# Kernel tuning notes

Measured on AMD Instinct MI355X. Metric: run time of the kernel, lower is better.

Reference implementation:

```python
import jax, jax.numpy as jnp
import numpy as np

K_DIM = 64  # contraction dim for scores; scale = 1/sqrt(K_DIM)


def setup_inputs() -> dict:
    key = jax.random.key(0)
    ks = jax.random.split(key, 8)
    B, T, L, D, H, E, V = 128, 16, 32, 256, 8, 64, 64
    return {
        "queries": jax.random.normal(ks[0], (B, T, L, D), dtype=jnp.float32),
        "keys": jax.random.normal(ks[1], (B, T, L, D), dtype=jnp.float32),
        "values": jax.random.normal(ks[2], (B, T, L, D), dtype=jnp.float32),
        "attn_mask": jax.random.uniform(ks[3], (B, B), dtype=jnp.float32),
        "Wq": jax.random.normal(ks[4], (D, H, E), dtype=jnp.float32) * 0.05,
        "Wk": jax.random.normal(ks[5], (D, H, E), dtype=jnp.float32) * 0.05,
        "Wv": jax.random.normal(ks[6], (D, H, V), dtype=jnp.float32) * 0.05,
        "w_head": jax.random.normal(ks[7], (H,), dtype=jnp.float32),
    }


def reference(queries, keys, values, attn_mask, Wq, Wk, Wv, w_head):
    # QKV projections (EinsumDense 'abcd,def->abcef', no bias): [b,t,l,h,e]
    Q = jnp.einsum('btld,dhe->btlhe', queries, Wq)
    K = jnp.einsum('btld,dhe->btlhe', keys, Wk)
    V = jnp.einsum('btld,dhe->btlhe', values, Wv)

    scale = 1.0 / jnp.sqrt(jnp.float32(K_DIM))
    # cross-batch attention scores: [t, l, h, B, b]
    scores = jnp.einsum('Btlhe,btlhe->tlhBb', Q, K) * scale
    # multiplicative mask, broadcast over trailing [B, b]
    scores = scores * attn_mask
    # Dropout is identity at inference (Keras Dropout, training=False)

    attn = jnp.einsum('tlhBb,btlhe->Bthle', jax.nn.softmax(scores, axis=-1), V)
    # head-mixing output ('bthle,h->btle'): [b, t, l, v_dim]
    attn_output = jnp.einsum('bthle,h->btle', attn, w_head)
    return (attn_output, scores)
```

## Files before the change

### kernel.cpp

```cpp
#include <hip/hip_runtime.h>
#include <hip/hip_bf16.h>


using bf16x8 = __attribute__((ext_vector_type(8))) __bf16;
using f32x4  = __attribute__((ext_vector_type(4))) float;

__device__ __forceinline__ f32x4 mfma16(bf16x8 a, bf16x8 b, f32x4 c) {
  return __builtin_amdgcn_mfma_f32_16x16x32_bf16(a, b, c, 0, 0, 0);
}

__global__ __launch_bounds__(512) void k0_wt(const float* __restrict__ Wq,
                                             const float* __restrict__ Wk,
                                             const float* __restrict__ Wv,
                                             __bf16* __restrict__ Wt) {
  int f   = blockIdx.x * 512 + threadIdx.x;
  int mat = f >> 14;
  int rem = f & 16383;
  int d8  = rem >> 9;
  int col = rem & 511;
  const float* W = (mat == 0) ? Wq : (mat == 1) ? Wk : Wv;
  bf16x8 v;
#pragma unroll
  for (int i = 0; i < 8; ++i) v[i] = (__bf16)W[(d8 * 8 + i) * 512 + col];
  *(bf16x8*)(Wt + mat * 131072 + col * 256 + d8 * 8) = v;
}

__global__ __launch_bounds__(512) void k1_proj(const float* __restrict__ xq,
                                               const float* __restrict__ xk,
                                               const float* __restrict__ xv,
                                               const __bf16* __restrict__ Wt,
                                               __bf16* __restrict__ qkv) {
  __shared__ char smem[65536];
  const int tid  = threadIdx.x;
  const int tl   = blockIdx.x;
  const int m    = blockIdx.y;
  const int lane = tid & 63, w = tid >> 6;
  const int lrow = lane & 15, lk = lane >> 4;
  const f32x4 z4 = {0.f, 0.f, 0.f, 0.f};

  const float* xm = (m == 0) ? xq : (m == 1) ? xk : xv;

#pragma unroll
  for (int i = 0; i < 8; ++i) {
    int c = i * 512 + tid;
    int row = c >> 5, sl = c & 31;
    const float* g = xm + (size_t)row * 131072 + (size_t)tl * 256 + sl * 8;
    float4 f0 = *(const float4*)g;
    float4 f1 = *(const float4*)(g + 4);
    bf16x8 v;
    v[0] = (__bf16)f0.x; v[1] = (__bf16)f0.y; v[2] = (__bf16)f0.z; v[3] = (__bf16)f0.w;
    v[4] = (__bf16)f1.x; v[5] = (__bf16)f1.y; v[6] = (__bf16)f1.z; v[7] = (__bf16)f1.w;
    *(bf16x8*)(smem + row * 512 + ((sl ^ (row & 7)) << 4)) = v;
  }
  __syncthreads();

  const int h = w;
  const __bf16* wbase = Wt + (size_t)(m * 512 + h * 64) * 256;
  __bf16* dst = qkv + (size_t)(tl * 8 + h) * 32768 + m * 8192;

  for (int rh = 0; rh < 2; ++rh) {
    f32x4 acc[4][4];
#pragma unroll
    for (int ri = 0; ri < 4; ++ri)
#pragma unroll
      for (int ci = 0; ci < 4; ++ci) acc[ri][ci] = z4;

#pragma unroll
    for (int kk = 0; kk < 8; ++kk) {
      int koff = lk * 16 + kk * 64;
      bf16x8 a[4], b[4];
#pragma unroll
      for (int ri = 0; ri < 4; ++ri) {
        int row = rh * 64 + ri * 16 + lrow;
        a[ri] = *(const bf16x8*)(smem + row * 512 + (koff ^ ((row & 7) << 4)));
      }
#pragma unroll
      for (int ci = 0; ci < 4; ++ci)
        b[ci] = *(const bf16x8*)(wbase + (ci * 16 + lrow) * 256 + kk * 32 + lk * 8);
#pragma unroll
      for (int ri = 0; ri < 4; ++ri)
#pragma unroll
        for (int ci = 0; ci < 4; ++ci)
          acc[ri][ci] = mfma16(a[ri], b[ci], acc[ri][ci]);
    }

#pragma unroll
    for (int ri = 0; ri < 4; ++ri)
#pragma unroll
      for (int ci = 0; ci < 4; ++ci)
#pragma unroll
        for (int r = 0; r < 4; ++r) {
          int brow = rh * 64 + ri * 16 + lk * 4 + r;
          int e    = ci * 16 + lrow;
          dst[brow * 64 + e] = (__bf16)acc[ri][ci][r];
        }
  }
}

__global__ __launch_bounds__(512) void k2_attn(const float* __restrict__ mask,
                                               const float* __restrict__ w_head,
                                               float* out_base) {
  __shared__ char smem[81920];
  const int tid  = threadIdx.x;
  const int tl   = blockIdx.x;
  const int lane = tid & 63, w = tid >> 6;
  const int lrow = lane & 15, lk = lane >> 4;
  const f32x4 z4 = {0.f, 0.f, 0.f, 0.f};

  float* scores = out_base + 4194304;

  float mreg[8][4];
#pragma unroll
  for (int ct = 0; ct < 8; ++ct)
#pragma unroll
    for (int r = 0; r < 4; ++r)
      mreg[ct][r] = mask[(w * 16 + lk * 4 + r) * 128 + ct * 16 + lrow];

  f32x4 oacc[4];
#pragma unroll
  for (int i = 0; i < 4; ++i) oacc[i] = z4;

  for (int h = 0; h < 8; ++h) {
    const __bf16* slot = (const __bf16*)scores + (size_t)(tl * 8 + h) * 32768;
    float wh = w_head[h];
    __syncthreads();
#pragma unroll
    for (int i = 0; i < 2; ++i) {
      int c = i * 512 + tid;
      int row = c >> 3, sl = c & 7;
      uint4 qv = *(const uint4*)(slot + row * 64 + sl * 8);
      *(uint4*)(smem + row * 128 + ((sl ^ (row & 7)) << 4)) = qv;
      uint4 kv = *(const uint4*)(slot + 8192 + row * 64 + sl * 8);
      *(uint4*)(smem + 16384 + row * 128 + ((sl ^ (row & 7)) << 4)) = kv;
      bf16x8 vv = *(const bf16x8*)(slot + 16384 + row * 64 + sl * 8);
#pragma unroll
      for (int j = 0; j < 8; ++j) {
        int e = sl * 8 + j;
        *(__bf16*)(smem + 32768 + e * 256 + ((row * 2) ^ ((e & 7) << 4))) = vv[j];
      }
    }
    __syncthreads();

    int arow = w * 16 + lrow;
    const char* qb = smem + arow * 128;
    int aswz = (arow & 7) << 4;
    bf16x8 a0 = *(const bf16x8*)(qb + ((lk * 16 + 0) ^ aswz));
    bf16x8 a1 = *(const bf16x8*)(qb + ((lk * 16 + 64) ^ aswz));
    f32x4 sacc[8];
#pragma unroll
    for (int ct = 0; ct < 8; ++ct) {
      int bcol = ct * 16 + lrow;
      const char* kb = smem + 16384 + bcol * 128;
      int bswz = (bcol & 7) << 4;
      bf16x8 b0 = *(const bf16x8*)(kb + ((lk * 16 + 0) ^ bswz));
      bf16x8 b1 = *(const bf16x8*)(kb + ((lk * 16 + 64) ^ bswz));
      sacc[ct] = mfma16(a0, b0, z4);
      sacc[ct] = mfma16(a1, b1, sacc[ct]);
    }

    float* srow = scores + (size_t)(tl * 8 + h) * 16384;
#pragma unroll
    for (int ct = 0; ct < 8; ++ct)
#pragma unroll
      for (int r = 0; r < 4; ++r) {
        float s = sacc[ct][r] * 0.125f * mreg[ct][r];
        sacc[ct][r] = s;
        srow[(w * 16 + lk * 4 + r) * 128 + ct * 16 + lrow] = s;
      }

#pragma unroll
    for (int r = 0; r < 4; ++r) {
      float mx = sacc[0][r];
#pragma unroll
      for (int ct = 1; ct < 8; ++ct) mx = fmaxf(mx, sacc[ct][r]);
      mx = fmaxf(mx, __shfl_xor(mx, 1));
      mx = fmaxf(mx, __shfl_xor(mx, 2));
      mx = fmaxf(mx, __shfl_xor(mx, 4));
      mx = fmaxf(mx, __shfl_xor(mx, 8));
      float sum = 0.f;
#pragma unroll
      for (int ct = 0; ct < 8; ++ct) {
        float p = __expf(sacc[ct][r] - mx);
        sacc[ct][r] = p;
        sum += p;
      }
      sum += __shfl_xor(sum, 1);
      sum += __shfl_xor(sum, 2);
      sum += __shfl_xor(sum, 4);
      sum += __shfl_xor(sum, 8);
      float fct = wh / sum;
      int row16 = lk * 4 + r;
      char* pb = smem + 49152 + w * 4096 + row16 * 256;
      int pswz = (row16 & 7) << 4;
#pragma unroll
      for (int ct = 0; ct < 8; ++ct) {
        int col = ct * 16 + lrow;
        *(__bf16*)(pb + ((col * 2) ^ pswz)) = (__bf16)(sacc[ct][r] * fct);
      }
    }

    const char* pab = smem + 49152 + w * 4096 + lrow * 256;
    int paswz = (lrow & 7) << 4;
    bf16x8 pa[4];
#pragma unroll
    for (int kk = 0; kk < 4; ++kk)
      pa[kk] = *(const bf16x8*)(pab + ((lk * 16 + kk * 64) ^ paswz));
#pragma unroll
    for (int ct2 = 0; ct2 < 4; ++ct2) {
      int ecol = ct2 * 16 + lrow;
      const char* vb = smem + 32768 + ecol * 256;
      int vswz = (ecol & 7) << 4;
#pragma unroll
      for (int kk = 0; kk < 4; ++kk) {
        bf16x8 b = *(const bf16x8*)(vb + ((lk * 16 + kk * 64) ^ vswz));
        oacc[ct2] = mfma16(pa[kk], b, oacc[ct2]);
      }
    }
  }

#pragma unroll
  for (int ct2 = 0; ct2 < 4; ++ct2)
#pragma unroll
    for (int r = 0; r < 4; ++r) {
      int brow = w * 16 + lk * 4 + r;
      int e    = ct2 * 16 + lrow;
      out_base[(size_t)(brow * 512 + tl) * 64 + e] = oacc[ct2][r];
    }
}

extern "C" void kernel_launch(void* const* d_in, const int* in_sizes, int n_in,
                              void* d_out, int out_size, void* d_ws, size_t ws_size,
                              hipStream_t stream) {
  const float* q    = (const float*)d_in[0];
  const float* k    = (const float*)d_in[1];
  const float* v    = (const float*)d_in[2];
  const float* mask = (const float*)d_in[3];
  const float* Wq   = (const float*)d_in[4];
  const float* Wk   = (const float*)d_in[5];
  const float* Wv   = (const float*)d_in[6];
  const float* wh   = (const float*)d_in[7];
  float* out = (float*)d_out;

  __bf16* Wt  = (__bf16*)out;
  __bf16* qkv = (__bf16*)(out + 4194304);

  hipLaunchKernelGGL(k0_wt,   dim3(96),       dim3(512), 0, stream, Wq, Wk, Wv, Wt);
  hipLaunchKernelGGL(k1_proj, dim3(512, 3),   dim3(512), 0, stream, q, k, v, Wt, qkv);
  hipLaunchKernelGGL(k2_attn, dim3(512),      dim3(512), 0, stream, mask, wh, out);
}
```

Before: 235.2 us.

## Store V pre-transposed and vectorize projection writes, shrink attention LDS

The projection kernel is templated per matrix. For Q/K it swaps the MFMA operand order so each lane writes four contiguous bf16 values in one store, and for V it writes the output already transposed (e-major). The attention kernel then loads V with vectorized 16-byte copies instead of scalar transposing stores into LDS, and reads Q fragments straight from global memory, which cuts LDS from 80KB to 64KB. The one 2D launch becomes three separate launches, adding launch overhead, and launch_bounds(512,4) is added as an occupancy hint.

After: 323.6 us. +37.6%, slower.

```diff
diff --git a/kernel.cpp b/kernel.cpp
--- a/kernel.cpp
+++ b/kernel.cpp
@@ -3,6 +3,7 @@
 
 
 using bf16x8 = __attribute__((ext_vector_type(8))) __bf16;
+using bf16x4 = __attribute__((ext_vector_type(4))) __bf16;
 using f32x4  = __attribute__((ext_vector_type(4))) float;
 
 __device__ __forceinline__ f32x4 mfma16(bf16x8 a, bf16x8 b, f32x4 c) {
@@ -25,20 +26,16 @@
   *(bf16x8*)(Wt + mat * 131072 + col * 256 + d8 * 8) = v;
 }
 
-__global__ __launch_bounds__(512) void k1_proj(const float* __restrict__ xq,
-                                               const float* __restrict__ xk,
-                                               const float* __restrict__ xv,
-                                               const __bf16* __restrict__ Wt,
-                                               __bf16* __restrict__ qkv) {
+template <int M>
+__global__ __launch_bounds__(512, 4) void k1_proj(const float* __restrict__ xm,
+                                                  const __bf16* __restrict__ Wt,
+                                                  __bf16* __restrict__ qkv) {
   __shared__ char smem[65536];
   const int tid  = threadIdx.x;
   const int tl   = blockIdx.x;
-  const int m    = blockIdx.y;
   const int lane = tid & 63, w = tid >> 6;
   const int lrow = lane & 15, lk = lane >> 4;
   const f32x4 z4 = {0.f, 0.f, 0.f, 0.f};
-
-  const float* xm = (m == 0) ? xq : (m == 1) ? xk : xv;
 
 #pragma unroll
   for (int i = 0; i < 8; ++i) {
@@ -55,52 +52,70 @@
   __syncthreads();
 
   const int h = w;
-  const __bf16* wbase = Wt + (size_t)(m * 512 + h * 64) * 256;
-  __bf16* dst = qkv + (size_t)(tl * 8 + h) * 32768 + m * 8192;
-
-  for (int rh = 0; rh < 2; ++rh) {
+  const __bf16* wbase = Wt + (size_t)(M * 512 + h * 64) * 256;
+  __bf16* dst = qkv + (size_t)(tl * 8 + h) * 32768 + M * 8192;
+
+  for (int bh = 0; bh < 2; ++bh) {
     f32x4 acc[4][4];
 #pragma unroll
-    for (int ri = 0; ri < 4; ++ri)
-#pragma unroll
-      for (int ci = 0; ci < 4; ++ci) acc[ri][ci] = z4;
+    for (int i = 0; i < 4; ++i)
+#pragma unroll
+      for (int j = 0; j < 4; ++j) acc[i][j] = z4;
 
 #pragma unroll
     for (int kk = 0; kk < 8; ++kk) {
-      int koff = lk * 16 + kk * 64;
-      bf16x8 a[4], b[4];
-#pragma unroll
-      for (int ri = 0; ri < 4; ++ri) {
-        int row = rh * 64 + ri * 16 + lrow;
-        a[ri] = *(const bf16x8*)(smem + row * 512 + (koff ^ ((row & 7) << 4)));
-      }
-#pragma unroll
-      for (int ci = 0; ci < 4; ++ci)
-        b[ci] = *(const bf16x8*)(wbase + (ci * 16 + lrow) * 256 + kk * 32 + lk * 8);
-#pragma unroll
-      for (int ri = 0; ri < 4; ++ri)
-#pragma unroll
-        for (int ci = 0; ci < 4; ++ci)
-          acc[ri][ci] = mfma16(a[ri], b[ci], acc[ri][ci]);
-    }
-
-#pragma unroll
-    for (int ri = 0; ri < 4; ++ri)
-#pragma unroll
-      for (int ci = 0; ci < 4; ++ci)
-#pragma unroll
-        for (int r = 0; r < 4; ++r) {
-          int brow = rh * 64 + ri * 16 + lk * 4 + r;
-          int e    = ci * 16 + lrow;
-          dst[brow * 64 + e] = (__bf16)acc[ri][ci][r];
+      bf16x8 xf[4], wf[4];
+#pragma unroll
+      for (int i = 0; i < 4; ++i) {
+        int row = bh * 64 + i * 16 + lrow;
+        xf[i] = *(const bf16x8*)(smem + row * 512 + ((kk * 64 + lk * 16) ^ ((row & 7) << 4)));
+        wf[i] = *(const bf16x8*)(wbase + (i * 16 + lrow) * 256 + kk * 32 + lk * 8);
+      }
+      if (M < 2) {
+#pragma unroll
+        for (int ei = 0; ei < 4; ++ei)
+#pragma unroll
+          for (int bi = 0; bi < 4; ++bi)
+            acc[ei][bi] = mfma16(wf[ei], xf[bi], acc[ei][bi]);
+      } else {
+#pragma unroll
+        for (int bi = 0; bi < 4; ++bi)
+#pragma unroll
+          for (int ei = 0; ei < 4; ++ei)
+            acc[bi][ei] = mfma16(xf[bi], wf[ei], acc[bi][ei]);
+      }
+    }
+
+    if (M < 2) {
+#pragma unroll
+      for (int ei = 0; ei < 4; ++ei)
+#pragma unroll
+        for (int bi = 0; bi < 4; ++bi) {
+          bf16x4 v;
+#pragma unroll
+          for (int r = 0; r < 4; ++r) v[r] = (__bf16)acc[ei][bi][r];
+          int b = bh * 64 + bi * 16 + lrow;
+          *(bf16x4*)(dst + b * 64 + ei * 16 + lk * 4) = v;
         }
+    } else {
+#pragma unroll
+      for (int bi = 0; bi < 4; ++bi)
+#pragma unroll
+        for (int ei = 0; ei < 4; ++ei) {
+          bf16x4 v;
+#pragma unroll
+          for (int r = 0; r < 4; ++r) v[r] = (__bf16)acc[bi][ei][r];
+          int e = ei * 16 + lrow;
+          *(bf16x4*)(dst + e * 128 + bh * 64 + bi * 16 + lk * 4) = v;
+        }
+    }
   }
 }
 
 __global__ __launch_bounds__(512) void k2_attn(const float* __restrict__ mask,
                                                const float* __restrict__ w_head,
                                                float* out_base) {
-  __shared__ char smem[81920];
+  __shared__ char smem[65536];
   const int tid  = threadIdx.x;
   const int tl   = blockIdx.x;
   const int lane = tid & 63, w = tid >> 6;
@@ -120,37 +135,33 @@
 #pragma unroll
   for (int i = 0; i < 4; ++i) oacc[i] = z4;
 
+  const int arow = w * 16 + lrow;
+
   for (int h = 0; h < 8; ++h) {
     const __bf16* slot = (const __bf16*)scores + (size_t)(tl * 8 + h) * 32768;
     float wh = w_head[h];
+
+    bf16x8 a0 = *(const bf16x8*)(slot + arow * 64 + lk * 8);
+    bf16x8 a1 = *(const bf16x8*)(slot + arow * 64 + 32 + lk * 8);
+
     __syncthreads();
 #pragma unroll
     for (int i = 0; i < 2; ++i) {
-      int c = i * 512 + tid;
-      int row = c >> 3, sl = c & 7;
-      uint4 qv = *(const uint4*)(slot + row * 64 + sl * 8);
-      *(uint4*)(smem + row * 128 + ((sl ^ (row & 7)) << 4)) = qv;
-      uint4 kv = *(const uint4*)(slot + 8192 + row * 64 + sl * 8);
-      *(uint4*)(smem + 16384 + row * 128 + ((sl ^ (row & 7)) << 4)) = kv;
-      bf16x8 vv = *(const bf16x8*)(slot + 16384 + row * 64 + sl * 8);
-#pragma unroll
-      for (int j = 0; j < 8; ++j) {
-        int e = sl * 8 + j;
-        *(__bf16*)(smem + 32768 + e * 256 + ((row * 2) ^ ((e & 7) << 4))) = vv[j];
-      }
+      int cc = i * 512 + tid;
+      int krow = cc >> 3, ks = cc & 7;
+      uint4 kv = *(const uint4*)(slot + 8192 + krow * 64 + ks * 8);
+      *(uint4*)(smem + krow * 128 + ((ks ^ (krow & 7)) << 4)) = kv;
+      int e = cc >> 4, vs = cc & 15;
+      uint4 vv = *(const uint4*)(slot + 16384 + e * 128 + vs * 8);
+      *(uint4*)(smem + 16384 + e * 256 + ((vs ^ (e & 7)) << 4)) = vv;
     }
     __syncthreads();
 
-    int arow = w * 16 + lrow;
-    const char* qb = smem + arow * 128;
-    int aswz = (arow & 7) << 4;
-    bf16x8 a0 = *(const bf16x8*)(qb + ((lk * 16 + 0) ^ aswz));
-    bf16x8 a1 = *(const bf16x8*)(qb + ((lk * 16 + 64) ^ aswz));
     f32x4 sacc[8];
 #pragma unroll
     for (int ct = 0; ct < 8; ++ct) {
       int bcol = ct * 16 + lrow;
-      const char* kb = smem + 16384 + bcol * 128;
+      const char* kb = smem + bcol * 128;
       int bswz = (bcol & 7) << 4;
       bf16x8 b0 = *(const bf16x8*)(kb + ((lk * 16 + 0) ^ bswz));
       bf16x8 b1 = *(const bf16x8*)(kb + ((lk * 16 + 64) ^ bswz));
@@ -190,7 +201,7 @@
       sum += __shfl_xor(sum, 8);
       float fct = wh / sum;
       int row16 = lk * 4 + r;
-      char* pb = smem + 49152 + w * 4096 + row16 * 256;
+      char* pb = smem + 32768 + w * 4096 + row16 * 256;
       int pswz = (row16 & 7) << 4;
 #pragma unroll
       for (int ct = 0; ct < 8; ++ct) {
@@ -199,7 +210,7 @@
       }
     }
 
-    const char* pab = smem + 49152 + w * 4096 + lrow * 256;
+    const char* pab = smem + 32768 + w * 4096 + lrow * 256;
     int paswz = (lrow & 7) << 4;
     bf16x8 pa[4];
 #pragma unroll
@@ -208,7 +219,7 @@
 #pragma unroll
     for (int ct2 = 0; ct2 < 4; ++ct2) {
       int ecol = ct2 * 16 + lrow;
-      const char* vb = smem + 32768 + ecol * 256;
+      const char* vb = smem + 16384 + ecol * 256;
       int vswz = (ecol & 7) << 4;
 #pragma unroll
       for (int kk = 0; kk < 4; ++kk) {
@@ -244,7 +255,9 @@
   __bf16* Wt  = (__bf16*)out;
   __bf16* qkv = (__bf16*)(out + 4194304);
 
-  hipLaunchKernelGGL(k0_wt,   dim3(96),       dim3(512), 0, stream, Wq, Wk, Wv, Wt);
-  hipLaunchKernelGGL(k1_proj, dim3(512, 3),   dim3(512), 0, stream, q, k, v, Wt, qkv);
-  hipLaunchKernelGGL(k2_attn, dim3(512),      dim3(512), 0, stream, mask, wh, out);
-}
+  hipLaunchKernelGGL(k0_wt,      dim3(96),  dim3(512), 0, stream, Wq, Wk, Wv, Wt);
+  hipLaunchKernelGGL(k1_proj<0>, dim3(512), dim3(512), 0, stream, q, Wt, qkv);
+  hipLaunchKernelGGL(k1_proj<1>, dim3(512), dim3(512), 0, stream, k, Wt, qkv);
+  hipLaunchKernelGGL(k1_proj<2>, dim3(512), dim3(512), 0, stream, v, Wt, qkv);
+  hipLaunchKernelGGL(k2_attn,    dim3(512), dim3(512), 0, stream, mask, wh, out);
+}
```
